# Optimization experiments

Measured on AMD Instinct MI355X. Metric: run time of the kernel, lower is better.

## Reference

```python
import jax, jax.numpy as jnp
import numpy as np

COMMITMENT_WEIGHT = 0.25
B, D, L, K = 131072, 256, 4, 1024


def setup_inputs() -> dict:
    key = jax.random.key(0)
    k1, k2 = jax.random.split(key)
    ze = jax.random.normal(k1, (B, D), dtype=jnp.float32)
    codebooks = jax.random.normal(k2, (L, K, D), dtype=jnp.float32) * 0.02
    return {"ze": ze, "codebooks": codebooks}


def reference(ze, codebooks):
    # Sequential residual VQ over L levels via lax.scan (carry = residual).
    def step(residual, codebook):
        # squared L2 distances [B, K] via ||r||^2 + ||c||^2 - 2 r.c
        dists = ((residual ** 2).sum(axis=1, keepdims=True)
                 + (codebook ** 2).sum(axis=1)[None, :]
                 - 2.0 * residual @ codebook.T)
        idx = jnp.argmin(dists, axis=1)           # [B]
        quantized = codebook[idx]                 # [B, D] embedding gather
        commit = jnp.mean((residual - jax.lax.stop_gradient(quantized)) ** 2)
        cb = jnp.mean((quantized - jax.lax.stop_gradient(residual)) ** 2)
        new_residual = residual - quantized
        return new_residual, (idx, quantized, new_residual, commit, cb)

    _, (idx_l, q_l, res_l, commits, cbs) = jax.lax.scan(step, ze, codebooks)

    indices = idx_l.T                              # [B, L]
    quantized_stack = jnp.transpose(q_l, (1, 0, 2))  # [B, L, D]
    quantized_sum_qspace = quantized_stack.sum(axis=1)  # [B, D]
    # straight-through estimator
    quantized_sum_qspace = ze + jax.lax.stop_gradient(quantized_sum_qspace - ze)
    quantized_sum = quantized_sum_qspace  # no output projection (quantizer_dim == input_dim)
    residual_states = jnp.concatenate([ze[None], res_l], axis=0)  # [L+1, B, D]

    commitment_loss = commits.mean()
    codebook_loss = cbs.mean()
    quantization_loss = COMMITMENT_WEIGHT * commitment_loss + codebook_loss

    return (indices, quantized_stack, quantized_sum, quantized_sum_qspace,
            residual_states, commitment_loss, codebook_loss, quantization_loss)
```

## Files before the change

kernel.cpp:

```cpp
#include <hip/hip_runtime.h>

#define Bsz 131072
#define Dd  256
#define Ll  4
#define Kk  1024
#define TB  32
#define NWG (Bsz / TB)
#define CAP 2048
#define MARGIN 0.05f

#define O_IDX   0ULL
#define O_QSTK  524288ULL
#define O_QSUM  (O_QSTK + (size_t)Bsz * Ll * Dd)
#define O_QSQ   (O_QSUM + (size_t)Bsz * Dd)
#define O_RES   (O_QSQ  + (size_t)Bsz * Dd)
#define O_LOSS  (O_RES  + (size_t)(Ll + 1) * Bsz * Dd)

#define WS_C2_OFF  16384
#define WS_CBH_OFF 32768

typedef short v8s __attribute__((ext_vector_type(8)));
typedef float v4f __attribute__((ext_vector_type(4)));

__device__ __forceinline__ unsigned short f2bf(float f) {
    unsigned u = __float_as_uint(f);
    return (unsigned short)((u + 0x7fffu + ((u >> 16) & 1u)) >> 16);
}

__device__ __forceinline__ float np_rowsum_sq(const float* a) {
    float blk[2];
    #pragma unroll
    for (int hb = 0; hb < 2; ++hb) {
        const float* p = a + hb * 128;
        float r8[8][4];
        #pragma unroll
        for (int j = 0; j < 8; ++j) {
            float4 x = *(const float4*)(p + 4 * j);
            r8[j][0] = __fmul_rn(x.x, x.x);
            r8[j][1] = __fmul_rn(x.y, x.y);
            r8[j][2] = __fmul_rn(x.z, x.z);
            r8[j][3] = __fmul_rn(x.w, x.w);
        }
        #pragma unroll
        for (int i = 32; i < 128; i += 32) {
            #pragma unroll
            for (int j = 0; j < 8; ++j) {
                float4 x = *(const float4*)(p + i + 4 * j);
                r8[j][0] = __fadd_rn(r8[j][0], __fmul_rn(x.x, x.x));
                r8[j][1] = __fadd_rn(r8[j][1], __fmul_rn(x.y, x.y));
                r8[j][2] = __fadd_rn(r8[j][2], __fmul_rn(x.z, x.z));
                r8[j][3] = __fadd_rn(r8[j][3], __fmul_rn(x.w, x.w));
            }
        }
        float wv[4];
        #pragma unroll
        for (int L = 0; L < 4; ++L) {
            wv[L] = __fadd_rn(
                __fadd_rn(__fadd_rn(r8[0][L], r8[1][L]), __fadd_rn(r8[2][L], r8[3][L])),
                __fadd_rn(__fadd_rn(r8[4][L], r8[5][L]), __fadd_rn(r8[6][L], r8[7][L])));
        }
        blk[hb] = __fadd_rn(__fadd_rn(wv[0], wv[1]), __fadd_rn(wv[2], wv[3]));
    }
    return __fadd_rn(blk[0], blk[1]);
}

__global__ void prep_kernel(const float* __restrict__ cbks, float* __restrict__ ws) {
    int t = blockIdx.x * 256 + threadIdx.x;
    if (t < Ll * Kk) ws[WS_C2_OFF + t] = np_rowsum_sq(cbks + (size_t)t * Dd);
}

__global__ void cvt_kernel(const float* __restrict__ cbks, float* __restrict__ ws) {
    unsigned short* cbh = (unsigned short*)(ws + WS_CBH_OFF);
    int i = (blockIdx.x * 256 + threadIdx.x) * 4;
    float4 x = *(const float4*)(cbks + i);
    ushort4 y;
    y.x = f2bf(x.x); y.y = f2bf(x.y); y.z = f2bf(x.z); y.w = f2bf(x.w);
    *(ushort4*)(cbh + i) = y;
}

__global__ __launch_bounds__(256, 2) void rvq_kernel(
    const float* __restrict__ ze, const float* __restrict__ cbks,
    float* __restrict__ out, float* __restrict__ ws)
{
    __shared__ float  rbuf[TB][Dd + 4];
    __shared__ unsigned short rb16[TB * Dd];
    __shared__ float  r2s[TB];
    __shared__ unsigned long long best64[TB];
    __shared__ float  mrun[4][TB];
    __shared__ int    clist[CAP];
    __shared__ int    ccount;
    __shared__ int    bidx[TB];
    __shared__ float  wssq[4];

    const int tid  = threadIdx.x;
    const int wg   = blockIdx.x;
    const int b0   = wg * TB;
    const int lane = tid & 63;
    const int w    = tid >> 6;
    const int lrow = lane & 15;
    const int lk   = lane >> 4;

    const float* c2  = ws + WS_C2_OFF;
    const unsigned short* cbh = (const unsigned short*)(ws + WS_CBH_OFF);

    for (int i = tid; i < TB * Dd / 4; i += 256) {
        int v  = i >> 6;
        int dp = (i & 63) << 2;
        float4 x = *(const float4*)(ze + (size_t)(b0 + v) * Dd + dp);
        *(float4*)&rbuf[v][dp] = x;
        *(float4*)(out + O_RES + (size_t)(b0 + v) * Dd + dp) = x;
    }
    __syncthreads();

    for (int l = 0; l < Ll; ++l) {
        if (tid < TB) { r2s[tid] = np_rowsum_sq(&rbuf[tid][0]); best64[tid] = ~0ull; }
        if (tid < 128) mrun[tid >> 5][tid & 31] = 1e30f;
        if (tid == 0) ccount = 0;
        for (int gi = tid; gi < TB * 32; gi += 256) {
            int v = gi >> 5, g = gi & 31;
            float4 x0 = *(const float4*)&rbuf[v][g * 8];
            float4 x1 = *(const float4*)&rbuf[v][g * 8 + 4];
            v8s o;
            o[0] = (short)f2bf(x0.x); o[1] = (short)f2bf(x0.y);
            o[2] = (short)f2bf(x0.z); o[3] = (short)f2bf(x0.w);
            o[4] = (short)f2bf(x1.x); o[5] = (short)f2bf(x1.y);
            o[6] = (short)f2bf(x1.z); o[7] = (short)f2bf(x1.w);
            *(v8s*)&rb16[v * Dd + ((g ^ (v & 7)) << 3)] = o;
        }
        __syncthreads();

        const unsigned short* cbh_l = cbh + (size_t)l * Kk * Dd;
        const float* c2l = c2 + l * Kk;
        const float* cb  = cbks + (size_t)l * Kk * Dd;

        const unsigned short* ap0 = &rb16[(size_t)lrow * Dd];
        const unsigned short* ap1 = &rb16[(size_t)(lrow + 16) * Dd];
        const int axor = lrow & 7;

        for (int sc = 0; sc < 4; ++sc) {
            const int cbase = w * 256 + sc * 64;
            v4f acc[2][4];
            #pragma unroll
            for (int rt = 0; rt < 2; ++rt)
                #pragma unroll
                for (int ct = 0; ct < 4; ++ct) acc[rt][ct] = (v4f)(0.f);

            const unsigned short* bp[4];
            #pragma unroll
            for (int ct = 0; ct < 4; ++ct)
                bp[ct] = cbh_l + (size_t)(cbase + ct * 16 + lrow) * Dd + lk * 8;

            #pragma unroll
            for (int ks = 0; ks < 8; ++ks) {
                int aoff = (((ks * 4 + lk) ^ axor) << 3);
                v8s a0 = *(const v8s*)(ap0 + aoff);
                v8s a1 = *(const v8s*)(ap1 + aoff);
                #pragma unroll
                for (int ct = 0; ct < 4; ++ct) {
                    v8s b = *(const v8s*)(bp[ct] + ks * 32);
                    acc[0][ct] = __builtin_amdgcn_mfma_f32_16x16x32_bf16(a0, b, acc[0][ct], 0, 0, 0);
                    acc[1][ct] = __builtin_amdgcn_mfma_f32_16x16x32_bf16(a1, b, acc[1][ct], 0, 0, 0);
                }
            }

            float c2v[4];
            #pragma unroll
            for (int ct = 0; ct < 4; ++ct) c2v[ct] = c2l[cbase + ct * 16 + lrow];

            #pragma unroll
            for (int rt = 0; rt < 2; ++rt) {
                #pragma unroll
                for (int reg = 0; reg < 4; ++reg) {
                    int row = rt * 16 + lk * 4 + reg;
                    float t0 = c2v[0] - 2.f * acc[rt][0][reg];
                    float t1 = c2v[1] - 2.f * acc[rt][1][reg];
                    float t2 = c2v[2] - 2.f * acc[rt][2][reg];
                    float t3 = c2v[3] - 2.f * acc[rt][3][reg];
                    float pm = fminf(fminf(t0, t1), fminf(t2, t3));
                    pm = fminf(pm, __shfl_xor(pm, 1));
                    pm = fminf(pm, __shfl_xor(pm, 2));
                    pm = fminf(pm, __shfl_xor(pm, 4));
                    pm = fminf(pm, __shfl_xor(pm, 8));
                    float nm = fminf(mrun[w][row], pm);
                    mrun[w][row] = nm;
                    float th = nm + MARGIN;
                    if (t0 < th) { int p = atomicAdd(&ccount, 1); if (p < CAP) clist[p] = (row << 10) | (cbase + 0 * 16 + lrow); }
                    if (t1 < th) { int p = atomicAdd(&ccount, 1); if (p < CAP) clist[p] = (row << 10) | (cbase + 1 * 16 + lrow); }
                    if (t2 < th) { int p = atomicAdd(&ccount, 1); if (p < CAP) clist[p] = (row << 10) | (cbase + 2 * 16 + lrow); }
                    if (t3 < th) { int p = atomicAdd(&ccount, 1); if (p < CAP) clist[p] = (row << 10) | (cbase + 3 * 16 + lrow); }
                }
            }
        }
        __syncthreads();

        {
            int cnt = ccount;
            int total = (cnt <= CAP) ? cnt : (TB * Kk);
            for (int ci = tid; ci < total; ci += 256) {
                int row, code;
                if (cnt <= CAP) { int rc = clist[ci]; row = rc >> 10; code = rc & 1023; }
                else            { row = ci >> 10; code = ci & 1023; }
                const float* cp = cb + (size_t)code * Dd;
                const float* rp = &rbuf[row][0];
                float a = 0.f;
                #pragma unroll 4
                for (int d = 0; d < Dd; d += 4) {
                    float4 cv = *(const float4*)(cp + d);
                    a = __fmaf_rn(rp[d + 0], cv.x, a);
                    a = __fmaf_rn(rp[d + 1], cv.y, a);
                    a = __fmaf_rn(rp[d + 2], cv.z, a);
                    a = __fmaf_rn(rp[d + 3], cv.w, a);
                }
                float s = __fsub_rn(__fadd_rn(r2s[row], c2l[code]), 2.0f * a);
                unsigned long long pk =
                    (((unsigned long long)__float_as_uint(s)) << 32) | (unsigned)code;
                atomicMin(&best64[row], pk);
            }
        }
        __syncthreads();

        if (tid < TB) {
            int code = (int)(best64[tid] & 0xffffffffu);
            bidx[tid] = code;
            out[O_IDX + (size_t)(b0 + tid) * Ll + l] = (float)code;
        }
        __syncthreads();

        float ssq = 0.f;
        for (int v = w * 8; v < w * 8 + 8; ++v) {
            int idx = bidx[v];
            const float4 q = *(const float4*)(cb + (size_t)idx * Dd + (lane << 2));
            float4 r = *(const float4*)&rbuf[v][lane << 2];
            float4 nr = make_float4(r.x - q.x, r.y - q.y, r.z - q.z, r.w - q.w);
            *(float4*)&rbuf[v][lane << 2] = nr;
            size_t gb = (size_t)(b0 + v);
            *(float4*)(out + O_QSTK + ((gb * Ll) + l) * Dd + (lane << 2)) = q;
            *(float4*)(out + O_RES + ((size_t)(l + 1) * Bsz + gb) * Dd + (lane << 2)) = nr;
            ssq += nr.x * nr.x + nr.y * nr.y + nr.z * nr.z + nr.w * nr.w;
        }
        #pragma unroll
        for (int m = 32; m; m >>= 1) ssq += __shfl_xor(ssq, m);
        if (lane == 0) wssq[w] = ssq;
        __syncthreads();
        if (tid == 0) ws[wg * 4 + l] = wssq[0] + wssq[1] + wssq[2] + wssq[3];
        __syncthreads();
    }

    for (int i = tid; i < TB * Dd / 4; i += 256) {
        int v  = i >> 6;
        int dp = (i & 63) << 2;
        size_t gb = (size_t)(b0 + v);
        float4 z = *(const float4*)(ze + gb * Dd + dp);
        float4 r = *(const float4*)&rbuf[v][dp];
        float4 qs = make_float4(z.x - r.x, z.y - r.y, z.z - r.z, z.w - r.w);
        *(float4*)(out + O_QSUM + gb * Dd + dp) = qs;
        float4 qq = make_float4(z.x + (qs.x - z.x), z.y + (qs.y - z.y),
                                z.z + (qs.z - z.z), z.w + (qs.w - z.w));
        *(float4*)(out + O_QSQ + gb * Dd + dp) = qq;
    }
}

__global__ void loss_kernel(const float* __restrict__ ws, float* __restrict__ out) {
    __shared__ float red[Ll * 4];
    int tid = threadIdx.x;
    int lane = tid & 63, w = tid >> 6;
    for (int l = 0; l < Ll; ++l) {
        float s = 0.f;
        for (int i = tid; i < NWG; i += 256) s += ws[i * 4 + l];
        #pragma unroll
        for (int m = 32; m; m >>= 1) s += __shfl_xor(s, m);
        if (lane == 0) red[l * 4 + w] = s;
    }
    __syncthreads();
    if (tid == 0) {
        float tot = 0.f;
        for (int l = 0; l < Ll; ++l)
            tot += red[l * 4 + 0] + red[l * 4 + 1] + red[l * 4 + 2] + red[l * 4 + 3];
        float cm = tot / (float)((size_t)Ll * Bsz * Dd);
        out[O_LOSS + 0] = cm;
        out[O_LOSS + 1] = cm;
        out[O_LOSS + 2] = 0.25f * cm + cm;
    }
}

extern "C" void kernel_launch(void* const* d_in, const int* in_sizes, int n_in,
                              void* d_out, int out_size, void* d_ws, size_t ws_size,
                              hipStream_t stream) {
    (void)in_sizes; (void)n_in; (void)out_size; (void)ws_size;
    const float* ze   = (const float*)d_in[0];
    const float* cbks = (const float*)d_in[1];
    float* out = (float*)d_out;
    float* ws  = (float*)d_ws;

    hipLaunchKernelGGL(prep_kernel, dim3(16), dim3(256), 0, stream, cbks, ws);
    hipLaunchKernelGGL(cvt_kernel, dim3(Ll * Kk * Dd / 1024), dim3(256), 0, stream, cbks, ws);
    hipLaunchKernelGGL(rvq_kernel, dim3(NWG), dim3(256), 0, stream, ze, cbks, out, ws);
    hipLaunchKernelGGL(loss_kernel, dim3(1), dim3(256), 0, stream, ws, out);
}
```

Measured before the change: 1.991 ms.

## Use 512-thread workgroups, split codebook across 8 waves, parallelize row norms

Doubles the workgroup to 512 threads so each of 8 waves scans 128 codes instead of 256, and unrolls the shortened code-chunk loop. The per-row squared-norm computation, previously done serially by 32 threads, is now spread across 16 lanes per row with shuffle reductions. The separate index-writeback step and one barrier are removed by reading best indices directly in the residual update. The larger block with launch_bounds(512,2) raises register pressure and may reduce occupancy, and the shuffle reduction order may not match the previous norm summation bit for bit.

```diff
diff --git a/kernel.cpp b/kernel.cpp
--- a/kernel.cpp
+++ b/kernel.cpp
@@ -6,6 +6,7 @@
 #define Kk  1024
 #define TB  32
 #define NWG (Bsz / TB)
+#define NT  512
 #define CAP 2048
 #define MARGIN 0.05f
 
@@ -78,7 +79,7 @@
     *(ushort4*)(cbh + i) = y;
 }
 
-__global__ __launch_bounds__(256, 2) void rvq_kernel(
+__global__ __launch_bounds__(NT, 2) void rvq_kernel(
     const float* __restrict__ ze, const float* __restrict__ cbks,
     float* __restrict__ out, float* __restrict__ ws)
 {
@@ -86,11 +87,10 @@
     __shared__ unsigned short rb16[TB * Dd];
     __shared__ float  r2s[TB];
     __shared__ unsigned long long best64[TB];
-    __shared__ float  mrun[4][TB];
+    __shared__ float  mrun[8][TB];
     __shared__ int    clist[CAP];
     __shared__ int    ccount;
-    __shared__ int    bidx[TB];
-    __shared__ float  wssq[4];
+    __shared__ float  wssq[8];
 
     const int tid  = threadIdx.x;
     const int wg   = blockIdx.x;
@@ -103,7 +103,7 @@
     const float* c2  = ws + WS_C2_OFF;
     const unsigned short* cbh = (const unsigned short*)(ws + WS_CBH_OFF);
 
-    for (int i = tid; i < TB * Dd / 4; i += 256) {
+    for (int i = tid; i < TB * Dd / 4; i += NT) {
         int v  = i >> 6;
         int dp = (i & 63) << 2;
         float4 x = *(const float4*)(ze + (size_t)(b0 + v) * Dd + dp);
@@ -113,10 +113,37 @@
     __syncthreads();
 
     for (int l = 0; l < Ll; ++l) {
-        if (tid < TB) { r2s[tid] = np_rowsum_sq(&rbuf[tid][0]); best64[tid] = ~0ull; }
-        if (tid < 128) mrun[tid >> 5][tid & 31] = 1e30f;
+        {
+            const int row = tid >> 4;
+            const int sub = tid & 15;
+            const int j   = sub & 7;
+            const int hb  = sub >> 3;
+            const float* p = &rbuf[row][hb * 128 + j * 4];
+            float4 x = *(const float4*)p;
+            float q0 = __fmul_rn(x.x, x.x), q1 = __fmul_rn(x.y, x.y);
+            float q2 = __fmul_rn(x.z, x.z), q3 = __fmul_rn(x.w, x.w);
+            #pragma unroll
+            for (int i = 32; i < 128; i += 32) {
+                float4 y = *(const float4*)(p + i);
+                q0 = __fadd_rn(q0, __fmul_rn(y.x, y.x));
+                q1 = __fadd_rn(q1, __fmul_rn(y.y, y.y));
+                q2 = __fadd_rn(q2, __fmul_rn(y.z, y.z));
+                q3 = __fadd_rn(q3, __fmul_rn(y.w, y.w));
+            }
+            #pragma unroll
+            for (int m = 1; m < 8; m <<= 1) {
+                q0 = __fadd_rn(q0, __shfl_xor(q0, m));
+                q1 = __fadd_rn(q1, __shfl_xor(q1, m));
+                q2 = __fadd_rn(q2, __shfl_xor(q2, m));
+                q3 = __fadd_rn(q3, __shfl_xor(q3, m));
+            }
+            float blk = __fadd_rn(__fadd_rn(q0, q1), __fadd_rn(q2, q3));
+            float tot = __fadd_rn(blk, __shfl_xor(blk, 8));
+            if (sub == 0) { r2s[row] = tot; best64[row] = ~0ull; }
+        }
+        if (tid < 256) mrun[tid >> 5][tid & 31] = 1e30f;
         if (tid == 0) ccount = 0;
-        for (int gi = tid; gi < TB * 32; gi += 256) {
+        for (int gi = tid; gi < TB * 32; gi += NT) {
             int v = gi >> 5, g = gi & 31;
             float4 x0 = *(const float4*)&rbuf[v][g * 8];
             float4 x1 = *(const float4*)&rbuf[v][g * 8 + 4];
@@ -137,8 +164,9 @@
         const unsigned short* ap1 = &rb16[(size_t)(lrow + 16) * Dd];
         const int axor = lrow & 7;
 
-        for (int sc = 0; sc < 4; ++sc) {
-            const int cbase = w * 256 + sc * 64;
+        #pragma unroll
+        for (int sc = 0; sc < 2; ++sc) {
+            const int cbase = w * 128 + sc * 64;
             v4f acc[2][4];
             #pragma unroll
             for (int rt = 0; rt < 2; ++rt)
@@ -196,7 +224,7 @@
         {
             int cnt = ccount;
             int total = (cnt <= CAP) ? cnt : (TB * Kk);
-            for (int ci = tid; ci < total; ci += 256) {
+            for (int ci = tid; ci < total; ci += NT) {
                 int row, code;
                 if (cnt <= CAP) { int rc = clist[ci]; row = rc >> 10; code = rc & 1023; }
                 else            { row = ci >> 10; code = ci & 1023; }
@@ -219,16 +247,10 @@
         }
         __syncthreads();
 
-        if (tid < TB) {
-            int code = (int)(best64[tid] & 0xffffffffu);
-            bidx[tid] = code;
-            out[O_IDX + (size_t)(b0 + tid) * Ll + l] = (float)code;
-        }
-        __syncthreads();
-
         float ssq = 0.f;
-        for (int v = w * 8; v < w * 8 + 8; ++v) {
-            int idx = bidx[v];
+        for (int v = w * 4; v < w * 4 + 4; ++v) {
+            int idx = (int)(best64[v] & 0xffffffffu);
+            if (lane == 0) out[O_IDX + (size_t)(b0 + v) * Ll + l] = (float)idx;
             const float4 q = *(const float4*)(cb + (size_t)idx * Dd + (lane << 2));
             float4 r = *(const float4*)&rbuf[v][lane << 2];
             float4 nr = make_float4(r.x - q.x, r.y - q.y, r.z - q.z, r.w - q.w);
@@ -242,11 +264,16 @@
         for (int m = 32; m; m >>= 1) ssq += __shfl_xor(ssq, m);
         if (lane == 0) wssq[w] = ssq;
         __syncthreads();
-        if (tid == 0) ws[wg * 4 + l] = wssq[0] + wssq[1] + wssq[2] + wssq[3];
-        __syncthreads();
-    }
-
-    for (int i = tid; i < TB * Dd / 4; i += 256) {
+        if (tid == 0) {
+            float s = 0.f;
+            #pragma unroll
+            for (int i = 0; i < 8; ++i) s += wssq[i];
+            ws[wg * 4 + l] = s;
+        }
+        __syncthreads();
+    }
+
+    for (int i = tid; i < TB * Dd / 4; i += NT) {
         int v  = i >> 6;
         int dp = (i & 63) << 2;
         size_t gb = (size_t)(b0 + v);
@@ -294,6 +321,6 @@
 
     hipLaunchKernelGGL(prep_kernel, dim3(16), dim3(256), 0, stream, cbks, ws);
     hipLaunchKernelGGL(cvt_kernel, dim3(Ll * Kk * Dd / 1024), dim3(256), 0, stream, cbks, ws);
-    hipLaunchKernelGGL(rvq_kernel, dim3(NWG), dim3(256), 0, stream, ze, cbks, out, ws);
+    hipLaunchKernelGGL(rvq_kernel, dim3(NWG), dim3(NT), 0, stream, ze, cbks, out, ws);
     hipLaunchKernelGGL(loss_kernel, dim3(1), dim3(256), 0, stream, ws, out);
 }
```

Measured after the change: 2.502 ms. 1.26x slower.

## Keep residual rows in registers per wave and drop block-level syncs

Applied to the files above, without the earlier changes.

Restructures the RVQ kernel so each wave owns 16 rows and holds their fp32 residual in registers in MFMA operand layout. This removes the shared-memory residual and bf16 staging buffers and all __syncthreads. Each wave now sweeps all 1024 codes itself, keeps its own candidate list and refines candidates by reading residual values through shuffles. The aim is less LDS traffic, no barriers and higher occupancy, at the cost of more codebook reads per row (each wave streams the whole codebook) and heavy register and shuffle pressure during refinement.

```diff
diff --git a/kernel.cpp b/kernel.cpp
--- a/kernel.cpp
+++ b/kernel.cpp
@@ -4,9 +4,10 @@
 #define Dd  256
 #define Ll  4
 #define Kk  1024
-#define TB  32
-#define NWG (Bsz / TB)
-#define CAP 2048
+#define RW  16
+#define NWG 2048
+#define NT  256
+#define CAPW 160
 #define MARGIN 0.05f
 
 #define O_IDX   0ULL
@@ -16,8 +17,8 @@
 #define O_RES   (O_QSQ  + (size_t)Bsz * Dd)
 #define O_LOSS  (O_RES  + (size_t)(Ll + 1) * Bsz * Dd)
 
-#define WS_C2_OFF  16384
-#define WS_CBH_OFF 32768
+#define WS_C2_OFF  32768
+#define WS_CBH_OFF 40960
 
 typedef short v8s __attribute__((ext_vector_type(8)));
 typedef float v4f __attribute__((ext_vector_type(4)));
@@ -78,185 +79,211 @@
     *(ushort4*)(cbh + i) = y;
 }
 
-__global__ __launch_bounds__(256, 2) void rvq_kernel(
+__global__ __launch_bounds__(NT, 3) void rvq_kernel(
     const float* __restrict__ ze, const float* __restrict__ cbks,
     float* __restrict__ out, float* __restrict__ ws)
 {
-    __shared__ float  rbuf[TB][Dd + 4];
-    __shared__ unsigned short rb16[TB * Dd];
-    __shared__ float  r2s[TB];
-    __shared__ unsigned long long best64[TB];
-    __shared__ float  mrun[4][TB];
-    __shared__ int    clist[CAP];
-    __shared__ int    ccount;
-    __shared__ int    bidx[TB];
-    __shared__ float  wssq[4];
+    __shared__ unsigned long long best64[4 * RW];
+    __shared__ int clist[4 * CAPW];
+    __shared__ int cc[4];
 
     const int tid  = threadIdx.x;
-    const int wg   = blockIdx.x;
-    const int b0   = wg * TB;
+    const int w    = tid >> 6;
     const int lane = tid & 63;
-    const int w    = tid >> 6;
-    const int lrow = lane & 15;
-    const int lk   = lane >> 4;
-
-    const float* c2  = ws + WS_C2_OFF;
+    const int r    = lane & 15;
+    const int hi   = lane >> 4;
+    const int rows0 = blockIdx.x * 64 + w * RW;
+    const size_t grow = (size_t)(rows0 + r);
+
+    const float* c2 = ws + WS_C2_OFF;
     const unsigned short* cbh = (const unsigned short*)(ws + WS_CBH_OFF);
 
-    for (int i = tid; i < TB * Dd / 4; i += 256) {
-        int v  = i >> 6;
-        int dp = (i & 63) << 2;
-        float4 x = *(const float4*)(ze + (size_t)(b0 + v) * Dd + dp);
-        *(float4*)&rbuf[v][dp] = x;
-        *(float4*)(out + O_RES + (size_t)(b0 + v) * Dd + dp) = x;
-    }
-    __syncthreads();
+    float res[8][8];
+
+    #pragma unroll
+    for (int ks = 0; ks < 8; ++ks) {
+        const int d0 = ks * 32 + hi * 8;
+        float4 z0 = *(const float4*)(ze + grow * Dd + d0);
+        float4 z1 = *(const float4*)(ze + grow * Dd + d0 + 4);
+        res[ks][0] = z0.x; res[ks][1] = z0.y; res[ks][2] = z0.z; res[ks][3] = z0.w;
+        res[ks][4] = z1.x; res[ks][5] = z1.y; res[ks][6] = z1.z; res[ks][7] = z1.w;
+        *(float4*)(out + O_RES + grow * Dd + d0)     = z0;
+        *(float4*)(out + O_RES + grow * Dd + d0 + 4) = z1;
+    }
 
     for (int l = 0; l < Ll; ++l) {
-        if (tid < TB) { r2s[tid] = np_rowsum_sq(&rbuf[tid][0]); best64[tid] = ~0ull; }
-        if (tid < 128) mrun[tid >> 5][tid & 31] = 1e30f;
-        if (tid == 0) ccount = 0;
-        for (int gi = tid; gi < TB * 32; gi += 256) {
-            int v = gi >> 5, g = gi & 31;
-            float4 x0 = *(const float4*)&rbuf[v][g * 8];
-            float4 x1 = *(const float4*)&rbuf[v][g * 8 + 4];
-            v8s o;
-            o[0] = (short)f2bf(x0.x); o[1] = (short)f2bf(x0.y);
-            o[2] = (short)f2bf(x0.z); o[3] = (short)f2bf(x0.w);
-            o[4] = (short)f2bf(x1.x); o[5] = (short)f2bf(x1.y);
-            o[6] = (short)f2bf(x1.z); o[7] = (short)f2bf(x1.w);
-            *(v8s*)&rb16[v * Dd + ((g ^ (v & 7)) << 3)] = o;
-        }
-        __syncthreads();
+        float blk[2];
+        #pragma unroll
+        for (int hb = 0; hb < 2; ++hb) {
+            float wv[4];
+            #pragma unroll
+            for (int L = 0; L < 4; ++L) {
+                float a0 = __fmul_rn(res[4*hb][L],     res[4*hb][L]);
+                float a1 = __fmul_rn(res[4*hb][4 + L], res[4*hb][4 + L]);
+                #pragma unroll
+                for (int m = 1; m < 4; ++m) {
+                    a0 = __fadd_rn(a0, __fmul_rn(res[4*hb+m][L],     res[4*hb+m][L]));
+                    a1 = __fadd_rn(a1, __fmul_rn(res[4*hb+m][4 + L], res[4*hb+m][4 + L]));
+                }
+                float p = __fadd_rn(a0, a1);
+                float q = __fadd_rn(p, __shfl_xor(p, 16));
+                wv[L]   = __fadd_rn(q, __shfl_xor(q, 32));
+            }
+            blk[hb] = __fadd_rn(__fadd_rn(wv[0], wv[1]), __fadd_rn(wv[2], wv[3]));
+        }
+        const float r2v = __fadd_rn(blk[0], blk[1]);
+
+        if (lane < RW) best64[w * RW + lane] = ~0ull;
+        if (lane == 0) cc[w] = 0;
+
+        v8s abf[8];
+        #pragma unroll
+        for (int ks = 0; ks < 8; ++ks) {
+            v8s t;
+            #pragma unroll
+            for (int j = 0; j < 8; ++j) t[j] = (short)f2bf(res[ks][j]);
+            abf[ks] = t;
+        }
 
         const unsigned short* cbh_l = cbh + (size_t)l * Kk * Dd;
         const float* c2l = c2 + l * Kk;
         const float* cb  = cbks + (size_t)l * Kk * Dd;
 
-        const unsigned short* ap0 = &rb16[(size_t)lrow * Dd];
-        const unsigned short* ap1 = &rb16[(size_t)(lrow + 16) * Dd];
-        const int axor = lrow & 7;
-
-        for (int sc = 0; sc < 4; ++sc) {
-            const int cbase = w * 256 + sc * 64;
-            v4f acc[2][4];
-            #pragma unroll
-            for (int rt = 0; rt < 2; ++rt)
-                #pragma unroll
-                for (int ct = 0; ct < 4; ++ct) acc[rt][ct] = (v4f)(0.f);
-
-            const unsigned short* bp[4];
-            #pragma unroll
-            for (int ct = 0; ct < 4; ++ct)
-                bp[ct] = cbh_l + (size_t)(cbase + ct * 16 + lrow) * Dd + lk * 8;
-
+        float mr[4] = {1e30f, 1e30f, 1e30f, 1e30f};
+        for (int ch = 0; ch < 16; ++ch) {
+            const int cbase = ch * 64;
+            v4f acc[4];
+            #pragma unroll
+            for (int ct = 0; ct < 4; ++ct) acc[ct] = (v4f)(0.f);
             #pragma unroll
             for (int ks = 0; ks < 8; ++ks) {
-                int aoff = (((ks * 4 + lk) ^ axor) << 3);
-                v8s a0 = *(const v8s*)(ap0 + aoff);
-                v8s a1 = *(const v8s*)(ap1 + aoff);
                 #pragma unroll
                 for (int ct = 0; ct < 4; ++ct) {
-                    v8s b = *(const v8s*)(bp[ct] + ks * 32);
-                    acc[0][ct] = __builtin_amdgcn_mfma_f32_16x16x32_bf16(a0, b, acc[0][ct], 0, 0, 0);
-                    acc[1][ct] = __builtin_amdgcn_mfma_f32_16x16x32_bf16(a1, b, acc[1][ct], 0, 0, 0);
-                }
-            }
-
+                    v8s b = *(const v8s*)(cbh_l + (size_t)(cbase + ct*16 + r) * Dd
+                                          + ks * 32 + hi * 8);
+                    acc[ct] = __builtin_amdgcn_mfma_f32_16x16x32_bf16(abf[ks], b, acc[ct], 0, 0, 0);
+                }
+            }
             float c2v[4];
             #pragma unroll
-            for (int ct = 0; ct < 4; ++ct) c2v[ct] = c2l[cbase + ct * 16 + lrow];
-
-            #pragma unroll
-            for (int rt = 0; rt < 2; ++rt) {
+            for (int ct = 0; ct < 4; ++ct) c2v[ct] = c2l[cbase + ct*16 + r];
+            #pragma unroll
+            for (int reg = 0; reg < 4; ++reg) {
+                const int lrow = hi * 4 + reg;
+                float t0 = c2v[0] - 2.f * acc[0][reg];
+                float t1 = c2v[1] - 2.f * acc[1][reg];
+                float t2 = c2v[2] - 2.f * acc[2][reg];
+                float t3 = c2v[3] - 2.f * acc[3][reg];
+                float pm = fminf(fminf(t0, t1), fminf(t2, t3));
+                pm = fminf(pm, __shfl_xor(pm, 1));
+                pm = fminf(pm, __shfl_xor(pm, 2));
+                pm = fminf(pm, __shfl_xor(pm, 4));
+                pm = fminf(pm, __shfl_xor(pm, 8));
+                float nm = fminf(mr[reg], pm);
+                mr[reg] = nm;
+                float th = nm + MARGIN;
+                if (t0 < th) { int p = atomicAdd(&cc[w], 1); if (p < CAPW) clist[w*CAPW+p] = (lrow << 10) | (cbase + r); }
+                if (t1 < th) { int p = atomicAdd(&cc[w], 1); if (p < CAPW) clist[w*CAPW+p] = (lrow << 10) | (cbase + 16 + r); }
+                if (t2 < th) { int p = atomicAdd(&cc[w], 1); if (p < CAPW) clist[w*CAPW+p] = (lrow << 10) | (cbase + 32 + r); }
+                if (t3 < th) { int p = atomicAdd(&cc[w], 1); if (p < CAPW) clist[w*CAPW+p] = (lrow << 10) | (cbase + 48 + r); }
+            }
+        }
+
+        {
+            int cnt = cc[w];
+            const bool ok = (cnt <= CAPW);
+            const int total = ok ? cnt : (RW * Kk);
+            for (int base = 0; base < total; base += 64) {
+                const int ci = base + lane;
+                int rr, code;
+                if (ok) {
+                    int rc = clist[w * CAPW + (ci < cnt ? ci : 0)];
+                    rr = rc >> 10; code = rc & 1023;
+                } else {
+                    rr = ci >> 10; code = ci & 1023;
+                }
+                const float* cp = cb + (size_t)code * Dd;
+                const float r2row = __shfl(r2v, rr);
+                float a = 0.f;
                 #pragma unroll
-                for (int reg = 0; reg < 4; ++reg) {
-                    int row = rt * 16 + lk * 4 + reg;
-                    float t0 = c2v[0] - 2.f * acc[rt][0][reg];
-                    float t1 = c2v[1] - 2.f * acc[rt][1][reg];
-                    float t2 = c2v[2] - 2.f * acc[rt][2][reg];
-                    float t3 = c2v[3] - 2.f * acc[rt][3][reg];
-                    float pm = fminf(fminf(t0, t1), fminf(t2, t3));
-                    pm = fminf(pm, __shfl_xor(pm, 1));
-                    pm = fminf(pm, __shfl_xor(pm, 2));
-                    pm = fminf(pm, __shfl_xor(pm, 4));
-                    pm = fminf(pm, __shfl_xor(pm, 8));
-                    float nm = fminf(mrun[w][row], pm);
-                    mrun[w][row] = nm;
-                    float th = nm + MARGIN;
-                    if (t0 < th) { int p = atomicAdd(&ccount, 1); if (p < CAP) clist[p] = (row << 10) | (cbase + 0 * 16 + lrow); }
-                    if (t1 < th) { int p = atomicAdd(&ccount, 1); if (p < CAP) clist[p] = (row << 10) | (cbase + 1 * 16 + lrow); }
-                    if (t2 < th) { int p = atomicAdd(&ccount, 1); if (p < CAP) clist[p] = (row << 10) | (cbase + 2 * 16 + lrow); }
-                    if (t3 < th) { int p = atomicAdd(&ccount, 1); if (p < CAP) clist[p] = (row << 10) | (cbase + 3 * 16 + lrow); }
-                }
-            }
-        }
-        __syncthreads();
-
-        {
-            int cnt = ccount;
-            int total = (cnt <= CAP) ? cnt : (TB * Kk);
-            for (int ci = tid; ci < total; ci += 256) {
-                int row, code;
-                if (cnt <= CAP) { int rc = clist[ci]; row = rc >> 10; code = rc & 1023; }
-                else            { row = ci >> 10; code = ci & 1023; }
-                const float* cp = cb + (size_t)code * Dd;
-                const float* rp = &rbuf[row][0];
-                float a = 0.f;
-                #pragma unroll 4
-                for (int d = 0; d < Dd; d += 4) {
-                    float4 cv = *(const float4*)(cp + d);
-                    a = __fmaf_rn(rp[d + 0], cv.x, a);
-                    a = __fmaf_rn(rp[d + 1], cv.y, a);
-                    a = __fmaf_rn(rp[d + 2], cv.z, a);
-                    a = __fmaf_rn(rp[d + 3], cv.w, a);
-                }
-                float s = __fsub_rn(__fadd_rn(r2s[row], c2l[code]), 2.0f * a);
-                unsigned long long pk =
-                    (((unsigned long long)__float_as_uint(s)) << 32) | (unsigned)code;
-                atomicMin(&best64[row], pk);
-            }
-        }
-        __syncthreads();
-
-        if (tid < TB) {
-            int code = (int)(best64[tid] & 0xffffffffu);
-            bidx[tid] = code;
-            out[O_IDX + (size_t)(b0 + tid) * Ll + l] = (float)code;
-        }
-        __syncthreads();
-
+                for (int ks = 0; ks < 8; ++ks) {
+                    #pragma unroll
+                    for (int hh = 0; hh < 4; ++hh) {
+                        const int src = rr + (hh << 4);
+                        float4 c0 = *(const float4*)(cp + ks * 32 + hh * 8);
+                        float4 c1 = *(const float4*)(cp + ks * 32 + hh * 8 + 4);
+                        a = __fmaf_rn(__shfl(res[ks][0], src), c0.x, a);
+                        a = __fmaf_rn(__shfl(res[ks][1], src), c0.y, a);
+                        a = __fmaf_rn(__shfl(res[ks][2], src), c0.z, a);
+                        a = __fmaf_rn(__shfl(res[ks][3], src), c0.w, a);
+                        a = __fmaf_rn(__shfl(res[ks][4], src), c1.x, a);
+                        a = __fmaf_rn(__shfl(res[ks][5], src), c1.y, a);
+                        a = __fmaf_rn(__shfl(res[ks][6], src), c1.z, a);
+                        a = __fmaf_rn(__shfl(res[ks][7], src), c1.w, a);
+                    }
+                }
+                float s = __fsub_rn(__fadd_rn(r2row, c2l[code]), 2.0f * a);
+                if (!ok || ci < cnt) {
+                    unsigned long long pk =
+                        (((unsigned long long)__float_as_uint(s)) << 32) | (unsigned)code;
+                    atomicMin(&best64[w * RW + rr], pk);
+                }
+            }
+        }
+
+        unsigned long long bb = best64[w * RW + r];
+        const int idx = (int)(bb & 0xffffffffu);
+        if (lane < RW)
+            out[O_IDX + (size_t)(rows0 + lane) * Ll + l] =
+                (float)(int)(best64[w * RW + lane] & 0xffffffffu);
+
+        const float* qp = cb + (size_t)idx * Dd;
         float ssq = 0.f;
-        for (int v = w * 8; v < w * 8 + 8; ++v) {
-            int idx = bidx[v];
-            const float4 q = *(const float4*)(cb + (size_t)idx * Dd + (lane << 2));
-            float4 r = *(const float4*)&rbuf[v][lane << 2];
-            float4 nr = make_float4(r.x - q.x, r.y - q.y, r.z - q.z, r.w - q.w);
-            *(float4*)&rbuf[v][lane << 2] = nr;
-            size_t gb = (size_t)(b0 + v);
-            *(float4*)(out + O_QSTK + ((gb * Ll) + l) * Dd + (lane << 2)) = q;
-            *(float4*)(out + O_RES + ((size_t)(l + 1) * Bsz + gb) * Dd + (lane << 2)) = nr;
-            ssq += nr.x * nr.x + nr.y * nr.y + nr.z * nr.z + nr.w * nr.w;
+        #pragma unroll
+        for (int ks = 0; ks < 8; ++ks) {
+            const int d0 = ks * 32 + hi * 8;
+            float4 q0 = *(const float4*)(qp + d0);
+            float4 q1 = *(const float4*)(qp + d0 + 4);
+            res[ks][0] = __fsub_rn(res[ks][0], q0.x);
+            res[ks][1] = __fsub_rn(res[ks][1], q0.y);
+            res[ks][2] = __fsub_rn(res[ks][2], q0.z);
+            res[ks][3] = __fsub_rn(res[ks][3], q0.w);
+            res[ks][4] = __fsub_rn(res[ks][4], q1.x);
+            res[ks][5] = __fsub_rn(res[ks][5], q1.y);
+            res[ks][6] = __fsub_rn(res[ks][6], q1.z);
+            res[ks][7] = __fsub_rn(res[ks][7], q1.w);
+            *(float4*)(out + O_QSTK + ((grow * Ll) + l) * Dd + d0)     = q0;
+            *(float4*)(out + O_QSTK + ((grow * Ll) + l) * Dd + d0 + 4) = q1;
+            float4 n0 = make_float4(res[ks][0], res[ks][1], res[ks][2], res[ks][3]);
+            float4 n1 = make_float4(res[ks][4], res[ks][5], res[ks][6], res[ks][7]);
+            *(float4*)(out + O_RES + ((size_t)(l + 1) * Bsz + grow) * Dd + d0)     = n0;
+            *(float4*)(out + O_RES + ((size_t)(l + 1) * Bsz + grow) * Dd + d0 + 4) = n1;
+            ssq += n0.x*n0.x + n0.y*n0.y + n0.z*n0.z + n0.w*n0.w
+                 + n1.x*n1.x + n1.y*n1.y + n1.z*n1.z + n1.w*n1.w;
         }
         #pragma unroll
         for (int m = 32; m; m >>= 1) ssq += __shfl_xor(ssq, m);
-        if (lane == 0) wssq[w] = ssq;
-        __syncthreads();
-        if (tid == 0) ws[wg * 4 + l] = wssq[0] + wssq[1] + wssq[2] + wssq[3];
-        __syncthreads();
-    }
-
-    for (int i = tid; i < TB * Dd / 4; i += 256) {
-        int v  = i >> 6;
-        int dp = (i & 63) << 2;
-        size_t gb = (size_t)(b0 + v);
-        float4 z = *(const float4*)(ze + gb * Dd + dp);
-        float4 r = *(const float4*)&rbuf[v][dp];
-        float4 qs = make_float4(z.x - r.x, z.y - r.y, z.z - r.z, z.w - r.w);
-        *(float4*)(out + O_QSUM + gb * Dd + dp) = qs;
-        float4 qq = make_float4(z.x + (qs.x - z.x), z.y + (qs.y - z.y),
-                                z.z + (qs.z - z.z), z.w + (qs.w - z.w));
-        *(float4*)(out + O_QSQ + gb * Dd + dp) = qq;
+        if (lane == 0)
+            ws[((size_t)blockIdx.x * 4 + w) * 4 + l] = ssq;
+    }
+
+    #pragma unroll
+    for (int ks = 0; ks < 8; ++ks) {
+        const int d0 = ks * 32 + hi * 8;
+        float4 z0 = *(const float4*)(ze + grow * Dd + d0);
+        float4 z1 = *(const float4*)(ze + grow * Dd + d0 + 4);
+        float4 qs0 = make_float4(z0.x - res[ks][0], z0.y - res[ks][1],
+                                 z0.z - res[ks][2], z0.w - res[ks][3]);
+        float4 qs1 = make_float4(z1.x - res[ks][4], z1.y - res[ks][5],
+                                 z1.z - res[ks][6], z1.w - res[ks][7]);
+        *(float4*)(out + O_QSUM + grow * Dd + d0)     = qs0;
+        *(float4*)(out + O_QSUM + grow * Dd + d0 + 4) = qs1;
+        float4 qq0 = make_float4(z0.x + (qs0.x - z0.x), z0.y + (qs0.y - z0.y),
+                                 z0.z + (qs0.z - z0.z), z0.w + (qs0.w - z0.w));
+        float4 qq1 = make_float4(z1.x + (qs1.x - z1.x), z1.y + (qs1.y - z1.y),
+                                 z1.z + (qs1.z - z1.z), z1.w + (qs1.w - z1.w));
+        *(float4*)(out + O_QSQ + grow * Dd + d0)     = qq0;
+        *(float4*)(out + O_QSQ + grow * Dd + d0 + 4) = qq1;
     }
 }
 
@@ -266,7 +293,7 @@
     int lane = tid & 63, w = tid >> 6;
     for (int l = 0; l < Ll; ++l) {
         float s = 0.f;
-        for (int i = tid; i < NWG; i += 256) s += ws[i * 4 + l];
+        for (int i = tid; i < NWG * 4; i += 256) s += ws[i * 4 + l];
         #pragma unroll
         for (int m = 32; m; m >>= 1) s += __shfl_xor(s, m);
         if (lane == 0) red[l * 4 + w] = s;
@@ -294,6 +321,6 @@
 
     hipLaunchKernelGGL(prep_kernel, dim3(16), dim3(256), 0, stream, cbks, ws);
     hipLaunchKernelGGL(cvt_kernel, dim3(Ll * Kk * Dd / 1024), dim3(256), 0, stream, cbks, ws);
-    hipLaunchKernelGGL(rvq_kernel, dim3(NWG), dim3(256), 0, stream, ze, cbks, out, ws);
+    hipLaunchKernelGGL(rvq_kernel, dim3(NWG), dim3(NT), 0, stream, ze, cbks, out, ws);
     hipLaunchKernelGGL(loss_kernel, dim3(1), dim3(256), 0, stream, ws, out);
 }
```

New measurement: 4.049 ms. 103% more time.
